# Performance work log

Measured on AMD Instinct MI355X. Metric: run time of the kernel, lower is better.

## Reference

```python
import jax, jax.numpy as jnp
import numpy as np

# --- static config (matches init_kwargs) ---
B = 2; HI = 60; WI = 60; T = 4; WS = 8; SHIFT = 4
C = 256; NH = 8; HD = C // NH; HID = 1024
P = HI * WI; N = T * P
PAD = (WS - HI % WS) % WS           # 4 -> pad 60 -> 64
HP = HI + PAD; WP = WI + PAD
NWH = HP // WS; NWW = WP // WS
L = WS * WS                          # 64 tokens per window
SCALE = HD ** -0.5

# relative position index [L, L] (constant)
_c = np.stack(np.meshgrid(np.arange(WS), np.arange(WS), indexing='ij')).reshape(2, -1)
_r = (_c[:, :, None] - _c[:, None, :]).transpose(1, 2, 0) + WS - 1
REL_IDX = jnp.asarray(_r[..., 0] * (2 * WS - 1) + _r[..., 1])

# per-window key padding mask [nWin, L] (True = padded token)
_b = np.zeros((HP, WP), bool); _b[HI:, :] = True; _b[:, WI:] = True
WIN_MASK = jnp.asarray(_b.reshape(NWH, WS, NWW, WS).transpose(0, 2, 1, 3).reshape(NWH * NWW, L))


def _ln(x, w, b):
    m = x.mean(-1, keepdims=True)
    v = jnp.square(x - m).mean(-1, keepdims=True)
    return (x - m) * jax.lax.rsqrt(v + 1e-5) * w + b


def _partition(x4):  # [Bm, HP, WP, C] -> [Bm*nWin, L, C]
    Bm = x4.shape[0]
    return x4.reshape(Bm, NWH, WS, NWW, WS, C).transpose(0, 1, 3, 2, 4, 5).reshape(Bm * NWH * NWW, L, C)


def _win_attn(xq, xkv, qw, qb, kw, kb, vw, vb, ow, ob, bias_table):
    Bm = B * T
    q4 = xq.reshape(Bm, HI, WI, C)
    k4 = xkv.reshape(Bm, HI, WI, C)
    q4 = jnp.roll(q4, (-SHIFT, -SHIFT), (1, 2))
    k4 = jnp.roll(k4, (-SHIFT, -SHIFT), (1, 2))
    pad = ((0, 0), (0, PAD), (0, PAD), (0, 0))
    q4 = jnp.pad(q4, pad); k4 = jnp.pad(k4, pad)
    q_win = _partition(q4)   # [Bw, L, C]
    kv_win = _partition(k4)
    q = (q_win @ qw.T + qb).reshape(-1, L, NH, HD)
    k = (kv_win @ kw.T + kb).reshape(-1, L, NH, HD)
    v = (kv_win @ vw.T + vb).reshape(-1, L, NH, HD)
    attn = jnp.einsum('bihd,bjhd->bhij', q, k) * SCALE
    attn = attn + bias_table[REL_IDX].transpose(2, 0, 1)[None]      # RPB [1,H,L,L]
    km = jnp.tile(WIN_MASK, (Bm, 1))                                  # [Bw, L]
    attn = jnp.where(km[:, None, None, :], -jnp.inf, attn)
    p = jax.nn.softmax(attn, axis=-1)
    o = jnp.einsum('bhij,bjhd->bihd', p, v).reshape(-1, L, C)
    o = o @ ow.T + ob
    y = o.reshape(Bm, NWH, NWW, WS, WS, C).transpose(0, 1, 3, 2, 4, 5).reshape(Bm, HP, WP, C)
    y = y[:, :HI, :WI, :]
    y = jnp.roll(y, (SHIFT, SHIFT), (1, 2))
    return y.reshape(B, N, C)


def reference(x, context, ln1_w, ln1_b, ln2_w, ln2_b, ln3_w, ln3_b, lnc_w, lnc_b,
              sa_q_w, sa_q_b, sa_k_w, sa_k_b, sa_v_w, sa_v_b, sa_o_w, sa_o_b, sa_bias,
              ca_q_w, ca_q_b, ca_k_w, ca_k_b, ca_v_w, ca_v_b, ca_o_w, ca_o_b, ca_bias,
              gamma1, gamma2, gamma_mlp, mlp_w1, mlp_b1, mlp_w2, mlp_b2):
    xn = _ln(x, ln1_w, ln1_b)
    y_s = _win_attn(xn, xn, sa_q_w, sa_q_b, sa_k_w, sa_k_b, sa_v_w, sa_v_b, sa_o_w, sa_o_b, sa_bias)
    x = x + gamma1 * y_s
    y_c = _win_attn(_ln(x, ln2_w, ln2_b), _ln(context, lnc_w, lnc_b),
                    ca_q_w, ca_q_b, ca_k_w, ca_k_b, ca_v_w, ca_v_b, ca_o_w, ca_o_b, ca_bias)
    x = x + gamma2 * y_c
    h = _ln(x, ln3_w, ln3_b)
    h = jax.nn.gelu(h @ mlp_w1.T + mlp_b1, approximate=False) @ mlp_w2.T + mlp_b2
    return x + gamma_mlp * h


def setup_inputs() -> dict:
    key = jax.random.key(0)
    ks = jax.random.split(key, 16)
    def w(k, shape, s=0.02):
        return jax.random.normal(k, shape, jnp.float32) * s
    inp = {}
    inp['x'] = jax.random.normal(ks[0], (B, N, C), jnp.float32)
    inp['context'] = jax.random.normal(ks[1], (B, N, C), jnp.float32)
    for nm in ['ln1', 'ln2', 'ln3', 'lnc']:
        inp[f'{nm}_w'] = jnp.ones((C,), jnp.float32)
        inp[f'{nm}_b'] = jnp.zeros((C,), jnp.float32)
    i = 2
    for pfx in ['sa', 'ca']:
        for pn in ['q', 'k', 'v', 'o']:
            inp[f'{pfx}_{pn}_w'] = w(ks[i], (C, C)); i += 1
            inp[f'{pfx}_{pn}_b'] = jnp.zeros((C,), jnp.float32)
        inp[f'{pfx}_bias'] = w(ks[i], ((2 * WS - 1) * (2 * WS - 1), NH)); i += 1
    inp['gamma1'] = jnp.ones((1,), jnp.float32)
    inp['gamma2'] = jnp.ones((1,), jnp.float32)
    inp['gamma_mlp'] = jnp.full((1,), 0.1, jnp.float32)
    inp['mlp_w1'] = w(ks[i], (HID, C)); i += 1
    inp['mlp_b1'] = jnp.zeros((HID,), jnp.float32)
    inp['mlp_w2'] = w(ks[i], (C, HID)); i += 1
    inp['mlp_b2'] = jnp.zeros((C,), jnp.float32)
    return inp
```

## Files before the change

### kernel.cpp

```cpp
#include <hip/hip_runtime.h>
#include <math.h>

#define BN    28800
#define CC    256
#define HIDN  1024
#define WINS  512
#define WROWS (WINS*64)
#define ATT_SCALE 0.1767766952966369f

typedef __bf16 bf16x8 __attribute__((ext_vector_type(8)));
typedef float  f32x4  __attribute__((ext_vector_type(4)));

__device__ __forceinline__ unsigned short f2bf(float f) {
    unsigned u = __float_as_uint(f);
    unsigned r = (u + 0x7FFFu + ((u >> 16) & 1u)) >> 16;
    return (unsigned short)r;
}
__device__ __forceinline__ float bf2f(unsigned short u) {
    return __uint_as_float((unsigned)u << 16);
}

__device__ __forceinline__ float gelu_f(float x) {
    float x3 = x * x * x;
    float e  = __expf(1.5957691216057308f * (x + 0.044715f * x3));
    float th = 1.0f - 2.0f * __builtin_amdgcn_rcpf(e + 1.0f);
    return 0.5f * x * (1.0f + th);
}

__device__ __forceinline__ void gl_lds16(const void* g, void* l) {
    __builtin_amdgcn_global_load_lds(
        (const __attribute__((address_space(1))) void*)g,
        (__attribute__((address_space(3))) void*)l, 16, 0, 0);
}

__global__ void ln_kernel(const float* __restrict__ x, const float* __restrict__ w,
                          const float* __restrict__ b, unsigned short* __restrict__ out, int ntok) {
    int tok  = (int)((blockIdx.x * blockDim.x + threadIdx.x) >> 6);
    int lane = threadIdx.x & 63;
    if (tok >= ntok) return;
    float4 v = reinterpret_cast<const float4*>(x + (size_t)tok * CC)[lane];
    float s  = v.x + v.y + v.z + v.w;
    float s2 = v.x*v.x + v.y*v.y + v.z*v.z + v.w*v.w;
#pragma unroll
    for (int off = 32; off >= 1; off >>= 1) {
        s  += __shfl_xor(s, off);
        s2 += __shfl_xor(s2, off);
    }
    float mean = s * (1.0f / CC);
    float var  = s2 * (1.0f / CC) - mean * mean;
    float rs   = rsqrtf(var + 1e-5f);
    float4 wv = reinterpret_cast<const float4*>(w)[lane];
    float4 bv = reinterpret_cast<const float4*>(b)[lane];
    ushort4 o;
    o.x = f2bf((v.x - mean) * rs * wv.x + bv.x);
    o.y = f2bf((v.y - mean) * rs * wv.y + bv.y);
    o.z = f2bf((v.z - mean) * rs * wv.z + bv.z);
    o.w = f2bf((v.w - mean) * rs * wv.w + bv.w);
    reinterpret_cast<ushort4*>(out + (size_t)tok * CC)[lane] = o;
}

__global__ void ln_gather(const float* __restrict__ x, const float* __restrict__ w,
                          const float* __restrict__ b, unsigned short* __restrict__ dst) {
    int row  = (int)((blockIdx.x * blockDim.x + threadIdx.x) >> 6);
    int lane = threadIdx.x & 63;
    if (row >= WROWS) return;
    int win = row >> 6, l = row & 63;
    int f   = win >> 6;
    int wih = (win >> 3) & 7, wiw = win & 7;
    int r = l >> 3, s = l & 7;
    int h = wih * 8 + r, wc = wiw * 8 + s;
    if (h >= 60 || wc >= 60) {
        ushort4 z = {0, 0, 0, 0};
        reinterpret_cast<ushort4*>(dst + (size_t)row * CC)[lane] = z;
        return;
    }
    int oh = (h + 4) % 60, ow = (wc + 4) % 60;
    size_t tok = (size_t)f * 3600 + (size_t)oh * 60 + ow;
    float4 v = reinterpret_cast<const float4*>(x + tok * CC)[lane];
    float sm  = v.x + v.y + v.z + v.w;
    float s2 = v.x*v.x + v.y*v.y + v.z*v.z + v.w*v.w;
#pragma unroll
    for (int off = 32; off >= 1; off >>= 1) {
        sm += __shfl_xor(sm, off);
        s2 += __shfl_xor(s2, off);
    }
    float mean = sm * (1.0f / CC);
    float var  = s2 * (1.0f / CC) - mean * mean;
    float rs   = rsqrtf(var + 1e-5f);
    float4 wv = reinterpret_cast<const float4*>(w)[lane];
    float4 bv = reinterpret_cast<const float4*>(b)[lane];
    ushort4 o;
    o.x = f2bf((v.x - mean) * rs * wv.x + bv.x);
    o.y = f2bf((v.y - mean) * rs * wv.y + bv.y);
    o.z = f2bf((v.z - mean) * rs * wv.z + bv.z);
    o.w = f2bf((v.w - mean) * rs * wv.w + bv.w);
    reinterpret_cast<ushort4*>(dst + (size_t)row * CC)[lane] = o;
}

template <bool GELU, int FUSE>
__global__ __launch_bounds__(512, 4) void gemm_wa(
        const unsigned short* __restrict__ Wt,
        const unsigned short* __restrict__ Act,
        const float* __restrict__ b0, const float* __restrict__ b1,
        const float* __restrict__ b2, const float* __restrict__ b3,
        unsigned short* __restrict__ o0, unsigned short* __restrict__ o1,
        unsigned short* __restrict__ o2, unsigned short* __restrict__ o3,
        int strideO, int vseg, int K,
        const float* __restrict__ xres, const float* __restrict__ gammap,
        float* __restrict__ fout) {
    __shared__ __align__(16) char pool[32768];
    unsigned short* A0 = (unsigned short*)pool;
    unsigned short* B0 = (unsigned short*)(pool + 8192);
    unsigned short* A1 = (unsigned short*)(pool + 16384);
    unsigned short* B1 = (unsigned short*)(pool + 24576);
    unsigned short* Cs = (unsigned short*)pool;

    const int t = threadIdx.x;
    const int w = t >> 6;
    const int l = t & 63;
    const int Mb = gridDim.x;
    int lin = blockIdx.y * Mb + blockIdx.x;
    int T = Mb * gridDim.y;
    int q = T >> 3, rr = T & 7;
    int xcd = lin & 7, slot = lin >> 3;
    int wid = (xcd < rr) ? (xcd * (q + 1) + slot)
                         : (rr * (q + 1) + (xcd - rr) * q + slot);
    const int m0 = (wid % Mb) * 128;
    const int n0 = (wid / Mb) * 128;

    const int wr = w >> 2, wc = w & 3;
    const int r = l & 15, g = l >> 4;
    const int sw = (r >> 1) & 3;
    const int gp = (g ^ sw) * 8;
    const int srow = t >> 2;
    const int sgl  = (t & 3) ^ ((srow >> 1) & 3);

    f32x4 acc[4][2];
#pragma unroll
    for (int i = 0; i < 4; ++i)
#pragma unroll
        for (int j = 0; j < 2; ++j) { acc[i][j][0]=0.f; acc[i][j][1]=0.f; acc[i][j][2]=0.f; acc[i][j][3]=0.f; }

#define STAGE(k0, dA, dB)                                                          \
    do {                                                                           \
        gl_lds16(Wt  + (size_t)(m0 + srow) * K + (k0) + sgl * 8, (char*)(dA) + w * 1024); \
        gl_lds16(Act + (size_t)(n0 + srow) * K + (k0) + sgl * 8, (char*)(dB) + w * 1024); \
    } while (0)

    STAGE(0,  A0, B0);
    STAGE(32, A1, B1);
    const int nt = K >> 5;
    for (int kt = 0; kt < nt; ++kt) {
        if (kt < nt - 1)
            asm volatile("s_waitcnt vmcnt(2)" ::: "memory");
        else
            asm volatile("s_waitcnt vmcnt(0)" ::: "memory");
        __builtin_amdgcn_s_barrier();
        __builtin_amdgcn_sched_barrier(0);
        const unsigned short* cA = (kt & 1) ? A1 : A0;
        const unsigned short* cB = (kt & 1) ? B1 : B0;
        bf16x8 af[4], bw[2];
#pragma unroll
        for (int m = 0; m < 4; ++m)
            af[m] = *reinterpret_cast<const bf16x8*>(&cA[(wr * 64 + m * 16 + r) * 32 + gp]);
#pragma unroll
        for (int n = 0; n < 2; ++n)
            bw[n] = *reinterpret_cast<const bf16x8*>(&cB[(wc * 32 + n * 16 + r) * 32 + gp]);
#pragma unroll
        for (int m = 0; m < 4; ++m)
#pragma unroll
            for (int n = 0; n < 2; ++n)
                acc[m][n] = __builtin_amdgcn_mfma_f32_16x16x32_bf16(af[m], bw[n], acc[m][n], 0, 0, 0);
        __builtin_amdgcn_sched_barrier(0);
        asm volatile("s_waitcnt lgkmcnt(0)" ::: "memory");
        __builtin_amdgcn_s_barrier();
        __builtin_amdgcn_sched_barrier(0);
        if (kt + 2 < nt) {
            unsigned short* sA = (kt & 1) ? A1 : A0;
            unsigned short* sB = (kt & 1) ? B1 : B0;
            STAGE((kt + 2) * 32, sA, sB);
        }
    }
#undef STAGE

    const int seg = m0 >> 8;
    const float* bp = (seg == 0) ? b0 : (seg == 1) ? b1 : (seg == 2) ? b2 : b3;
    unsigned short* op = (seg == 0) ? o0 : (seg == 1) ? o1 : (seg == 2) ? o2 : o3;
    const int chseg = m0 & 255;

    if (FUSE == 0 && seg == vseg) {
#pragma unroll
        for (int m = 0; m < 4; ++m) {
            const int ch0 = chseg + wr * 64 + m * 16 + g * 4;
            float4 b4 = *reinterpret_cast<const float4*>(bp + ch0);
            const float bb[4] = {b4.x, b4.y, b4.z, b4.w};
#pragma unroll
            for (int n = 0; n < 2; ++n) {
                const int tok = n0 + wc * 32 + n * 16 + r;
#pragma unroll
                for (int j = 0; j < 4; ++j)
                    op[(size_t)(ch0 + j) * 32768 + tok] = f2bf(acc[m][n][j] + bb[j]);
            }
        }
        return;
    }

#pragma unroll
    for (int m = 0; m < 4; ++m) {
        const int ch0 = wr * 64 + m * 16 + g * 4;
        float4 b4 = *reinterpret_cast<const float4*>(bp + chseg + ch0);
        const float bb[4] = {b4.x, b4.y, b4.z, b4.w};
#pragma unroll
        for (int n = 0; n < 2; ++n) {
            const int tok_l = wc * 32 + n * 16 + r;
            float cv[4];
#pragma unroll
            for (int j = 0; j < 4; ++j) {
                cv[j] = acc[m][n][j] + bb[j];
                if (GELU) cv[j] = gelu_f(cv[j]);
            }
            ushort4 pk;
            pk.x = f2bf(cv[0]); pk.y = f2bf(cv[1]); pk.z = f2bf(cv[2]); pk.w = f2bf(cv[3]);
            int gran = (ch0 >> 2) ^ ((tok_l & 15) << 1);
            reinterpret_cast<ushort4*>(Cs)[tok_l * 32 + gran] = pk;
        }
    }
    __syncthreads();
    const int u = t & 15, trow = t >> 4;
    if (FUSE == 0) {
#pragma unroll
        for (int it = 0; it < 4; ++it) {
            int tok_l = it * 32 + trow;
            int up = u ^ (tok_l & 15);
            uint4 v = reinterpret_cast<const uint4*>(Cs)[tok_l * 16 + up];
            *reinterpret_cast<uint4*>(op + (size_t)(n0 + tok_l) * strideO + chseg + u * 8) = v;
        }
    } else {
        const float gsc = gammap[0];
#pragma unroll
        for (int it = 0; it < 4; ++it) {
            int tok_l = it * 32 + trow;
            int wrow = n0 + tok_l;
            int tok;
            if (FUSE == 1) {
                int win = wrow >> 6, l2 = wrow & 63;
                int f = win >> 6, wih = (win >> 3) & 7, wiw = win & 7;
                int r2 = l2 >> 3, s2 = l2 & 7;
                int h = wih * 8 + r2, wcol = wiw * 8 + s2;
                if (h >= 60 || wcol >= 60) continue;
                int oh = h + 4; if (oh >= 60) oh -= 60;
                int ow = wcol + 4; if (ow >= 60) ow -= 60;
                tok = f * 3600 + oh * 60 + ow;
            } else {
                tok = wrow;
            }
            int up = u ^ (tok_l & 15);
            uint4 v = reinterpret_cast<const uint4*>(Cs)[tok_l * 16 + up];
            const unsigned short* pu = (const unsigned short*)&v;
            const float* xr = xres + (size_t)tok * CC + chseg + u * 8;
            float4 xa = *reinterpret_cast<const float4*>(xr);
            float4 xb = *reinterpret_cast<const float4*>(xr + 4);
            float4 oa, ob;
            oa.x = xa.x + gsc * bf2f(pu[0]);
            oa.y = xa.y + gsc * bf2f(pu[1]);
            oa.z = xa.z + gsc * bf2f(pu[2]);
            oa.w = xa.w + gsc * bf2f(pu[3]);
            ob.x = xb.x + gsc * bf2f(pu[4]);
            ob.y = xb.y + gsc * bf2f(pu[5]);
            ob.z = xb.z + gsc * bf2f(pu[6]);
            ob.w = xb.w + gsc * bf2f(pu[7]);
            float* fo = fout + (size_t)tok * CC + chseg + u * 8;
            *reinterpret_cast<float4*>(fo) = oa;
            *reinterpret_cast<float4*>(fo + 4) = ob;
        }
    }
}

__global__ void expand_bias(const float* __restrict__ sa, const float* __restrict__ ca,
                            float* __restrict__ dst) {
    int e = (int)(blockIdx.x * blockDim.x + threadIdx.x);
    const float* src = (e < 16384) ? sa : ca;
    int e2 = e & 16383;
    int h = e2 >> 12, ij = e2 & 4095, i = ij >> 6, j = ij & 63;
    int ri = i >> 3, si = i & 7, rj = j >> 3, sj = j & 7;
    dst[e] = src[((ri - rj + 7) * 15 + (si - sj + 7)) * 8 + h];
}

__global__ __launch_bounds__(256) void attn_mfma(
        const unsigned short* __restrict__ Q,
        const unsigned short* __restrict__ K,
        const unsigned short* __restrict__ VT,
        const float* __restrict__ biasx,
        unsigned short* __restrict__ AO) {
    __shared__ __align__(16) unsigned short Pl[4][64 * 64];
    const int t = threadIdx.x;
    const int w = t >> 6, l = t & 63;
    const int win = blockIdx.x >> 1;
    const int h   = (blockIdx.x & 1) * 4 + w;
    const int c = l & 15, g = l >> 4;
    const int wih = (win >> 3) & 7, wiw = win & 7;
    const size_t qkbase = (size_t)win * 64 * CC + (size_t)h * 32;

    bf16x8 ka[4], qb[4];
#pragma unroll
    for (int mj = 0; mj < 4; ++mj)
        ka[mj] = *reinterpret_cast<const bf16x8*>(K + qkbase + (size_t)(mj * 16 + c) * CC + g * 8);
#pragma unroll
    for (int ni = 0; ni < 4; ++ni)
        qb[ni] = *reinterpret_cast<const bf16x8*>(Q + qkbase + (size_t)(ni * 16 + c) * CC + g * 8);
    f32x4 s[4][4];
#pragma unroll
    for (int mj = 0; mj < 4; ++mj)
#pragma unroll
        for (int ni = 0; ni < 4; ++ni) { s[mj][ni][0]=0.f; s[mj][ni][1]=0.f; s[mj][ni][2]=0.f; s[mj][ni][3]=0.f; }
#pragma unroll
    for (int mj = 0; mj < 4; ++mj)
#pragma unroll
        for (int ni = 0; ni < 4; ++ni)
            s[mj][ni] = __builtin_amdgcn_mfma_f32_16x16x32_bf16(ka[mj], qb[ni], s[mj][ni], 0, 0, 0);

    const float* bx = biasx + h * 4096;
    const bool modd = (wiw == 7) && (g & 1);
#pragma unroll
    for (int mj = 0; mj < 4; ++mj) {
        const bool mmj = (wih == 7) && (mj >= 2);
#pragma unroll
        for (int ni = 0; ni < 4; ++ni) {
            float4 b4 = *reinterpret_cast<const float4*>(bx + (ni * 16 + c) * 64 + mj * 16 + g * 4);
            const float bb[4] = {b4.x, b4.y, b4.z, b4.w};
#pragma unroll
            for (int jj = 0; jj < 4; ++jj) {
                float v = s[mj][ni][jj] * ATT_SCALE + bb[jj];
                s[mj][ni][jj] = (mmj || modd) ? -1e30f : v;
            }
        }
    }

#pragma unroll
    for (int ni = 0; ni < 4; ++ni) {
        float mx = -1e30f;
#pragma unroll
        for (int mj = 0; mj < 4; ++mj)
#pragma unroll
            for (int jj = 0; jj < 4; ++jj) mx = fmaxf(mx, s[mj][ni][jj]);
        mx = fmaxf(mx, __shfl_xor(mx, 16));
        mx = fmaxf(mx, __shfl_xor(mx, 32));
        float sum = 0.f;
#pragma unroll
        for (int mj = 0; mj < 4; ++mj)
#pragma unroll
            for (int jj = 0; jj < 4; ++jj) {
                float p = __expf(s[mj][ni][jj] - mx);
                s[mj][ni][jj] = p;
                sum += p;
            }
        sum += __shfl_xor(sum, 16);
        sum += __shfl_xor(sum, 32);
        float rinv = __builtin_amdgcn_rcpf(sum);
        const int i  = ni * 16 + c;
        const int ik = i & 7;
#pragma unroll
        for (int mj = 0; mj < 4; ++mj) {
            ushort4 pk;
            pk.x = f2bf(s[mj][ni][0] * rinv);
            pk.y = f2bf(s[mj][ni][1] * rinv);
            pk.z = f2bf(s[mj][ni][2] * rinv);
            pk.w = f2bf(s[mj][ni][3] * rinv);
            int chunk = (mj * 2 + (g >> 1)) ^ ik;
            *reinterpret_cast<ushort4*>((char*)&Pl[w][0] + i * 128 + chunk * 16 + (g & 1) * 8) = pk;
        }
    }

    bf16x8 vb[2][2];
#pragma unroll
    for (int nd = 0; nd < 2; ++nd)
#pragma unroll
        for (int kt = 0; kt < 2; ++kt)
            vb[nd][kt] = *reinterpret_cast<const bf16x8*>(
                VT + (size_t)(h * 32 + nd * 16 + c) * 32768 + win * 64 + kt * 32 + g * 8);
    f32x4 o[4][2];
#pragma unroll
    for (int mi = 0; mi < 4; ++mi)
#pragma unroll
        for (int nd = 0; nd < 2; ++nd) { o[mi][nd][0]=0.f; o[mi][nd][1]=0.f; o[mi][nd][2]=0.f; o[mi][nd][3]=0.f; }
#pragma unroll
    for (int mi = 0; mi < 4; ++mi) {
        const int i  = mi * 16 + c;
        const int ik = i & 7;
#pragma unroll
        for (int kt = 0; kt < 2; ++kt) {
            int chunk = (kt * 4 + g) ^ ik;
            bf16x8 pa = *reinterpret_cast<const bf16x8*>((char*)&Pl[w][0] + i * 128 + chunk * 16);
#pragma unroll
            for (int nd = 0; nd < 2; ++nd)
                o[mi][nd] = __builtin_amdgcn_mfma_f32_16x16x32_bf16(pa, vb[nd][kt], o[mi][nd], 0, 0, 0);
        }
    }

    unsigned short* aop = AO + qkbase;
#pragma unroll
    for (int mi = 0; mi < 4; ++mi)
#pragma unroll
        for (int nd = 0; nd < 2; ++nd)
#pragma unroll
            for (int jj = 0; jj < 4; ++jj)
                aop[(size_t)(mi * 16 + g * 4 + jj) * CC + nd * 16 + c] = f2bf(o[mi][nd][jj]);
}

__global__ void cvt_all(const float* s0, const float* s1, const float* s2, const float* s3,
                        const float* s4, const float* s5, const float* s6, const float* s7,
                        const float* s8, const float* s9, unsigned short* __restrict__ dst) {
    const float* srcs[10] = {s0, s1, s2, s3, s4, s5, s6, s7, s8, s9};
    int blk = blockIdx.x;
    int wi = (blk < 512) ? (blk >> 6) : (blk < 768 ? 8 : 9);
    size_t start = (wi < 8) ? (size_t)wi * 65536 : (wi == 8 ? (size_t)524288 : (size_t)786432);
    size_t gidx = (size_t)blk * 1024 + (size_t)threadIdx.x * 4;
    float4 v = *reinterpret_cast<const float4*>(srcs[wi] + (gidx - start));
    ushort4 o;
    o.x = f2bf(v.x); o.y = f2bf(v.y); o.z = f2bf(v.z); o.w = f2bf(v.w);
    *reinterpret_cast<ushort4*>(dst + gidx) = o;
}

extern "C" void kernel_launch(void* const* d_in, const int* in_sizes, int n_in,
                              void* d_out, int out_size, void* d_ws, size_t ws_size,
                              hipStream_t stream) {
    const float* x    = (const float*)d_in[0];
    const float* ctx  = (const float*)d_in[1];
    const float* ln1w = (const float*)d_in[2];
    const float* ln1b = (const float*)d_in[3];
    const float* ln2w = (const float*)d_in[4];
    const float* ln2b = (const float*)d_in[5];
    const float* ln3w = (const float*)d_in[6];
    const float* ln3b = (const float*)d_in[7];
    const float* lncw = (const float*)d_in[8];
    const float* lncb = (const float*)d_in[9];
    const float* saqw = (const float*)d_in[10];
    const float* saqb = (const float*)d_in[11];
    const float* sakw = (const float*)d_in[12];
    const float* sakb = (const float*)d_in[13];
    const float* savw = (const float*)d_in[14];
    const float* savb = (const float*)d_in[15];
    const float* saow = (const float*)d_in[16];
    const float* saob = (const float*)d_in[17];
    const float* sabias = (const float*)d_in[18];
    const float* caqw = (const float*)d_in[19];
    const float* caqb = (const float*)d_in[20];
    const float* cakw = (const float*)d_in[21];
    const float* cakb = (const float*)d_in[22];
    const float* cavw = (const float*)d_in[23];
    const float* cavb = (const float*)d_in[24];
    const float* caow = (const float*)d_in[25];
    const float* caob = (const float*)d_in[26];
    const float* cabias = (const float*)d_in[27];
    const float* gamma1 = (const float*)d_in[28];
    const float* gamma2 = (const float*)d_in[29];
    const float* gammam = (const float*)d_in[30];
    const float* mw1 = (const float*)d_in[31];
    const float* mb1 = (const float*)d_in[32];
    const float* mw2 = (const float*)d_in[33];
    const float* mb2 = (const float*)d_in[34];

    float* ws = (float*)d_ws;
    unsigned short* LNbf = (unsigned short*)(ws);
    unsigned short* Gq   = (unsigned short*)(ws + 3686400);
    unsigned short* Gkv  = (unsigned short*)(ws + 7880704);
    unsigned short* Qbf  = (unsigned short*)(ws + 12075008);
    unsigned short* Kbf  = (unsigned short*)(ws + 16269312);
    unsigned short* VTbf = (unsigned short*)(ws + 20463616);
    float* X1  = ws + 28852224;
    unsigned short* Wp = (unsigned short*)(ws + 36225024);
    float* biasx = ws + 36749312;
    unsigned short* AObf = Gq;
    unsigned short* H1bf = Qbf;

    unsigned short* w_saqkv = Wp;
    unsigned short* w_sao   = Wp + 196608;
    unsigned short* w_caq   = Wp + 262144;
    unsigned short* w_cakv  = Wp + 327680;
    unsigned short* w_cao   = Wp + 458752;
    unsigned short* w_m1    = Wp + 524288;
    unsigned short* w_m2    = Wp + 786432;

    float* OUT = (float*)d_out;

    dim3 blk(256);
    dim3 blk512(512);
    dim3 gLN(BN / 4);
    dim3 gGather(WROWS / 4);
    dim3 gAttn(WINS * 2);

    cvt_all<<<dim3(1024), blk, 0, stream>>>(saqw, sakw, savw, saow, caqw, cakw, cavw, caow, mw1, mw2, Wp);
    expand_bias<<<dim3(128), blk, 0, stream>>>(sabias, cabias, biasx);

    ln_gather<<<gGather, blk, 0, stream>>>(x, ln1w, ln1b, Gq);
    gemm_wa<false,0><<<dim3(6, 256), blk512, 0, stream>>>(w_saqkv, Gq, saqb, sakb, savb, savb,
                                                          Qbf, Kbf, VTbf, VTbf, CC, 2, CC,
                                                          nullptr, nullptr, nullptr);
    attn_mfma<<<gAttn, blk, 0, stream>>>(Qbf, Kbf, VTbf, biasx, AObf);
    gemm_wa<false,1><<<dim3(2, 256), blk512, 0, stream>>>(w_sao, AObf, saob, saob, saob, saob,
                                                          Qbf, Qbf, Qbf, Qbf, CC, -1, CC,
                                                          x, gamma1, X1);
    ln_gather<<<gGather, blk, 0, stream>>>(X1, ln2w, ln2b, Gq);
    ln_gather<<<gGather, blk, 0, stream>>>(ctx, lncw, lncb, Gkv);
    gemm_wa<false,0><<<dim3(2, 256), blk512, 0, stream>>>(w_caq, Gq, caqb, caqb, caqb, caqb,
                                                          Qbf, Qbf, Qbf, Qbf, CC, -1, CC,
                                                          nullptr, nullptr, nullptr);
    gemm_wa<false,0><<<dim3(4, 256), blk512, 0, stream>>>(w_cakv, Gkv, cakb, cavb, cavb, cavb,
                                                          Kbf, VTbf, VTbf, VTbf, CC, 1, CC,
                                                          nullptr, nullptr, nullptr);
    attn_mfma<<<gAttn, blk, 0, stream>>>(Qbf, Kbf, VTbf, biasx + 16384, AObf);
    gemm_wa<false,1><<<dim3(2, 256), blk512, 0, stream>>>(w_cao, AObf, caob, caob, caob, caob,
                                                          Qbf, Qbf, Qbf, Qbf, CC, -1, CC,
                                                          X1, gamma2, X1);
    ln_kernel<<<gLN, blk, 0, stream>>>(X1, ln3w, ln3b, LNbf, BN);
    gemm_wa<true,0><<<dim3(8, 225), blk512, 0, stream>>>(w_m1, LNbf, mb1, mb1 + 256, mb1 + 512, mb1 + 768,
                                                         H1bf, H1bf + 256, H1bf + 512, H1bf + 768,
                                                         HIDN, -1, CC, nullptr, nullptr, nullptr);
    gemm_wa<false,2><<<dim3(2, 225), blk512, 0, stream>>>(w_m2, H1bf, mb2, mb2, mb2, mb2,
                                                         Qbf, Qbf, Qbf, Qbf, CC, -1, HIDN,
                                                         X1, gammam, OUT);
}
```

Before: 240.5 us.

## Triple-buffer GEMM LDS stages to drop second barrier per k-step

Grows the shared-memory staging pool from two to three buffers and rotates through them. With three buffers, the prefetch for step k+2 writes into a buffer no wave is still reading, so the second lgkmcnt wait and barrier inside each k-iteration are removed. The MFMA block is also wrapped in s_setprio to favour the math waves, and a __syncthreads is added before the epilogue reuses the pool. The cost is 48KB of LDS per block, which may lower occupancy from the launch-bound target of 4 blocks per CU.

After: 243.2 us. About the same (+1.1%).

```diff
diff --git a/kernel.cpp b/kernel.cpp
--- a/kernel.cpp
+++ b/kernel.cpp
@@ -108,11 +108,7 @@
         int strideO, int vseg, int K,
         const float* __restrict__ xres, const float* __restrict__ gammap,
         float* __restrict__ fout) {
-    __shared__ __align__(16) char pool[32768];
-    unsigned short* A0 = (unsigned short*)pool;
-    unsigned short* B0 = (unsigned short*)(pool + 8192);
-    unsigned short* A1 = (unsigned short*)(pool + 16384);
-    unsigned short* B1 = (unsigned short*)(pool + 24576);
+    __shared__ __align__(16) char pool[49152];
     unsigned short* Cs = (unsigned short*)pool;
 
     const int t = threadIdx.x;
@@ -141,14 +137,20 @@
 #pragma unroll
         for (int j = 0; j < 2; ++j) { acc[i][j][0]=0.f; acc[i][j][1]=0.f; acc[i][j][2]=0.f; acc[i][j][3]=0.f; }
 
-#define STAGE(k0, dA, dB)                                                          \
+#define STAGE(k0, buf)                                                             \
     do {                                                                           \
-        gl_lds16(Wt  + (size_t)(m0 + srow) * K + (k0) + sgl * 8, (char*)(dA) + w * 1024); \
-        gl_lds16(Act + (size_t)(n0 + srow) * K + (k0) + sgl * 8, (char*)(dB) + w * 1024); \
+        gl_lds16(Wt  + (size_t)(m0 + srow) * K + (k0) + sgl * 8,                   \
+                 pool + (buf) * 16384 + w * 1024);                                 \
+        gl_lds16(Act + (size_t)(n0 + srow) * K + (k0) + sgl * 8,                   \
+                 pool + (buf) * 16384 + 8192 + w * 1024);                          \
     } while (0)
 
-    STAGE(0,  A0, B0);
-    STAGE(32, A1, B1);
+    STAGE(0, 0);
+    STAGE(32, 1);
+    const unsigned short* pA0 = (const unsigned short*)(pool);
+    const unsigned short* pA1 = (const unsigned short*)(pool + 16384);
+    const unsigned short* pA2 = (const unsigned short*)(pool + 32768);
+    int sbuf = 2;
     const int nt = K >> 5;
     for (int kt = 0; kt < nt; ++kt) {
         if (kt < nt - 1)
@@ -157,8 +159,8 @@
             asm volatile("s_waitcnt vmcnt(0)" ::: "memory");
         __builtin_amdgcn_s_barrier();
         __builtin_amdgcn_sched_barrier(0);
-        const unsigned short* cA = (kt & 1) ? A1 : A0;
-        const unsigned short* cB = (kt & 1) ? B1 : B0;
+        const unsigned short* cA = pA0;
+        const unsigned short* cB = pA0 + 4096;
         bf16x8 af[4], bw[2];
 #pragma unroll
         for (int m = 0; m < 4; ++m)
@@ -166,20 +168,18 @@
 #pragma unroll
         for (int n = 0; n < 2; ++n)
             bw[n] = *reinterpret_cast<const bf16x8*>(&cB[(wc * 32 + n * 16 + r) * 32 + gp]);
+        __builtin_amdgcn_s_setprio(1);
 #pragma unroll
         for (int m = 0; m < 4; ++m)
 #pragma unroll
             for (int n = 0; n < 2; ++n)
                 acc[m][n] = __builtin_amdgcn_mfma_f32_16x16x32_bf16(af[m], bw[n], acc[m][n], 0, 0, 0);
-        __builtin_amdgcn_sched_barrier(0);
-        asm volatile("s_waitcnt lgkmcnt(0)" ::: "memory");
-        __builtin_amdgcn_s_barrier();
-        __builtin_amdgcn_sched_barrier(0);
+        __builtin_amdgcn_s_setprio(0);
         if (kt + 2 < nt) {
-            unsigned short* sA = (kt & 1) ? A1 : A0;
-            unsigned short* sB = (kt & 1) ? B1 : B0;
-            STAGE((kt + 2) * 32, sA, sB);
-        }
+            STAGE((kt + 2) * 32, sbuf);
+            sbuf = (sbuf == 2) ? 0 : sbuf + 1;
+        }
+        const unsigned short* tmp = pA0; pA0 = pA1; pA1 = pA2; pA2 = tmp;
     }
 #undef STAGE
 
@@ -205,6 +205,7 @@
         return;
     }
 
+    __syncthreads();
 #pragma unroll
     for (int m = 0; m < 4; ++m) {
         const int ch0 = wr * 64 + m * 16 + g * 4;
```
